# Optimization experiments

Hardware: AMD Instinct MI355X
Metric: run time of the kernel (lower is better)

The kernel has to match this reference:

```python
import jax, jax.numpy as jnp
import numpy as np

B, N, D, H = 512, 64, 3, 128


def setup_inputs() -> dict:
    key = jax.random.key(0)
    ks = jax.random.split(key, 7)
    s1 = 1.0 / np.sqrt(6.0)
    s2 = 1.0 / np.sqrt(float(H))
    return {
        "pos_scaled": jax.random.normal(ks[0], (B, N, D), dtype=jnp.float32),
        "W1": jax.random.normal(ks[1], (6, H), dtype=jnp.float32) * s1,
        "b1": jax.random.normal(ks[2], (H,), dtype=jnp.float32) * 0.01,
        "W2": jax.random.normal(ks[3], (H, H), dtype=jnp.float32) * s2,
        "b2": jax.random.normal(ks[4], (H,), dtype=jnp.float32) * 0.01,
        "W3": jax.random.normal(ks[5], (H, 1), dtype=jnp.float32) * s2,
        "b3": jax.random.normal(ks[6], (1,), dtype=jnp.float32) * 0.01,
    }


def _features(dist):
    # dist: [B, N, N, 1]
    inv_r = 1.0 / jnp.maximum(dist, 0.5)
    inv6 = inv_r ** 6
    return jnp.concatenate(
        [dist, inv_r, inv6, inv6 * inv6, inv6 * inv_r, inv6 * inv6 * inv_r], axis=-1
    )  # [B, N, N, 6]


def reference(pos_scaled, W1, b1, W2, b2, W3, b3):
    # all-pairs displacement: [B, N, N, D]
    diff = pos_scaled[:, :, None, :] - pos_scaled[:, None, :, :]
    sq = jnp.sum(diff * diff, axis=-1, keepdims=True)  # [B, N, N, 1]
    # safe sqrt (grad-safe at 0; forward value identical)
    dist = jnp.sqrt(jnp.where(sq > 0, sq, 1.0))
    dist = jnp.where(sq > 0, dist, 0.0)

    feat = _features(dist)  # [B, N, N, 6]
    h = jnp.tanh(feat @ W1 + b1)
    h = jnp.tanh(h @ W2 + b2)
    mag = h @ W3 + b3  # [B, N, N, 1]

    n = pos_scaled.shape[1]
    mask = (~jnp.eye(n, dtype=bool))[None, :, :, None]  # off-diagonal pairs
    direction = diff / jnp.maximum(dist, 0.01)
    pair_forces = jnp.where(mask, mag * direction, 0.0)
    return jnp.sum(pair_forces, axis=2)  # [B, N, D]
```

## Files before the change

kernel.cpp:

```cpp
#include <hip/hip_runtime.h>
#include <hip/hip_bf16.h>
#include <math.h>


#define NFINE   16384
#define NCOARSE 8192
#define ENTRIES 128
#define NBUILD  ((NFINE + NCOARSE) / ENTRIES)

typedef __attribute__((ext_vector_type(8))) short bf16x8;
typedef __attribute__((ext_vector_type(4))) float f32x4;
typedef __attribute__((ext_vector_type(8))) unsigned short ushort8_t;

__device__ __forceinline__ float fast_tanh(float x) {
    float e = __expf(2.0f * x);
    return 1.0f - 2.0f * __builtin_amdgcn_rcpf(e + 1.0f);
}

__device__ __forceinline__ unsigned short f2bf(float x) {
    __hip_bfloat16 h = __float2bfloat16(x);
    return *reinterpret_cast<unsigned short*>(&h);
}

__global__ __launch_bounds__(256) void build_table(
    const float* __restrict__ W1, const float* __restrict__ b1,
    const float* __restrict__ W2, const float* __restrict__ b2,
    const float* __restrict__ W3, const float* __restrict__ b3,
    float* __restrict__ tabF, float* __restrict__ tabC) {
    __shared__ __attribute__((aligned(16))) float sW1[6 * 128];
    __shared__ __attribute__((aligned(16))) float sb1[128], sb2[128], sW3[128];
    __shared__ __attribute__((aligned(16))) unsigned short sW2T[128][136];

    const int t = threadIdx.x;

    if (t < 128) { sb1[t] = b1[t]; sb2[t] = b2[t]; sW3[t] = W3[t]; }
    for (int i = t; i < 768; i += 256) sW1[i] = W1[i];

    {
        int q = t & 63, c = t >> 6;
        const float* r0 = W2 + (2 * q) * 128 + c * 32;
        const float* r1 = r0 + 128;
#pragma unroll
        for (int m = 0; m < 8; ++m) {
            float4 a = *reinterpret_cast<const float4*>(r0 + 4 * m);
            float4 b = *reinterpret_cast<const float4*>(r1 + 4 * m);
            int n = c * 32 + 4 * m;
            *reinterpret_cast<ushort2*>(&sW2T[n + 0][2 * q]) = make_ushort2(f2bf(a.x), f2bf(b.x));
            *reinterpret_cast<ushort2*>(&sW2T[n + 1][2 * q]) = make_ushort2(f2bf(a.y), f2bf(b.y));
            *reinterpret_cast<ushort2*>(&sW2T[n + 2][2 * q]) = make_ushort2(f2bf(a.z), f2bf(b.z));
            *reinterpret_cast<ushort2*>(&sW2T[n + 3][2 * q]) = make_ushort2(f2bf(a.w), f2bf(b.w));
        }
    }

    int eb = blockIdx.x * ENTRIES;
    float dd; float* tp; int lo;
    if (eb < NFINE) { dd = 2.0f / (float)NFINE;    tp = tabF; lo = eb; }
    else            { dd = 16.0f / (float)NCOARSE; tp = tabC; lo = eb - NFINE; }

    const int w  = t >> 6;
    const int l  = t & 63;
    const int lg = l >> 4;
    const int lr = l & 15;

    __syncthreads();

    const float b3v = b3[0];

#pragma unroll
    for (int et = 0; et < 2; ++et) {
        const int e = et * 64 + w * 16 + lr;
        float d = (float)(lo + e) * dd;
        float inv_r = 1.0f / fmaxf(d, 0.5f);
        float inv2  = inv_r * inv_r;
        float inv6  = inv2 * inv2 * inv2;
        float inv12 = inv6 * inv6;
        float ft[6] = {d, inv_r, inv6, inv12, inv6 * inv_r, inv12 * inv_r};

        bf16x8 afr[4];
#pragma unroll
        for (int kt = 0; kt < 4; ++kt) {
            int c0 = kt * 32 + lg * 8;
            float ac[8], wv[8];
            *reinterpret_cast<float4*>(&ac[0]) = *reinterpret_cast<const float4*>(&sb1[c0]);
            *reinterpret_cast<float4*>(&ac[4]) = *reinterpret_cast<const float4*>(&sb1[c0 + 4]);
#pragma unroll
            for (int k = 0; k < 6; ++k) {
                *reinterpret_cast<float4*>(&wv[0]) = *reinterpret_cast<const float4*>(&sW1[k * 128 + c0]);
                *reinterpret_cast<float4*>(&wv[4]) = *reinterpret_cast<const float4*>(&sW1[k * 128 + c0 + 4]);
#pragma unroll
                for (int j = 0; j < 8; ++j) ac[j] = fmaf(ft[k], wv[j], ac[j]);
            }
            ushort8_t pk;
#pragma unroll
            for (int j = 0; j < 8; ++j) pk[j] = f2bf(fast_tanh(ac[j]));
            afr[kt] = *reinterpret_cast<bf16x8*>(&pk);
        }

        float part[4] = {0.f, 0.f, 0.f, 0.f};
#pragma unroll
        for (int nt = 0; nt < 8; ++nt) {
            f32x4 acc = {0.f, 0.f, 0.f, 0.f};
#pragma unroll
            for (int kt = 0; kt < 4; ++kt) {
                bf16x8 bfr = *reinterpret_cast<const bf16x8*>(&sW2T[nt * 16 + lr][kt * 32 + lg * 8]);
                acc = __builtin_amdgcn_mfma_f32_16x16x32_bf16(afr[kt], bfr, acc, 0, 0, 0);
            }
            float b2v = sb2[nt * 16 + lr];
            float w3v = sW3[nt * 16 + lr];
#pragma unroll
            for (int r = 0; r < 4; ++r)
                part[r] = fmaf(fast_tanh(acc[r] + b2v), w3v, part[r]);
        }
#pragma unroll
        for (int s = 1; s < 16; s <<= 1) {
#pragma unroll
            for (int r = 0; r < 4; ++r) part[r] += __shfl_xor(part[r], s);
        }
        if (lr == 0) {
            int ebase = et * 64 + w * 16 + lg * 4;
#pragma unroll
            for (int r = 0; r < 4; ++r) {
                int ee = lo + ebase + r;
                float dr = (float)ee * dd;
                tp[ee] = (part[r] + b3v) / fmaxf(dr, 0.01f);
            }
        }
    }
}

__global__ __launch_bounds__(256) void force_kernel(
    const float* __restrict__ pos, const float* __restrict__ tabF,
    const float* __restrict__ tabC, float* __restrict__ out) {
    __shared__ float sp[192];
    int b = blockIdx.x;
    int t = threadIdx.x;
    if (t < 192) sp[t] = pos[b * 192 + t];
    __syncthreads();

    int i  = t >> 2;
    int j0 = (t & 3) * 16;
    float xi = sp[i * 3 + 0], yi = sp[i * 3 + 1], zi = sp[i * 3 + 2];
    float fx = 0.f, fy = 0.f, fz = 0.f;
#pragma unroll
    for (int jj = 0; jj < 16; ++jj) {
        int j = j0 + jj;
        float dx = xi - sp[j * 3 + 0];
        float dy = yi - sp[j * 3 + 1];
        float dz = zi - sp[j * 3 + 2];
        float sq = fmaf(dx, dx, fmaf(dy, dy, dz * dz));
        float dist = sqrtf(sq);

        bool fine = dist < 2.0f;
        const float* tb = fine ? tabF : tabC;
        float scale = fine ? ((float)NFINE / 2.0f) : ((float)NCOARSE / 16.0f);
        int tmax = fine ? NFINE : NCOARSE;
        float tpos = dist * scale;
        int i0 = min((int)tpos, tmax - 2);
        float fr = tpos - (float)i0;
        float g0 = tb[i0], g1 = tb[i0 + 1];
        float g = fmaf(fr, g1 - g0, g0);
        if (j == i) g = 0.0f;

        fx = fmaf(g, dx, fx);
        fy = fmaf(g, dy, fy);
        fz = fmaf(g, dz, fz);
    }
    fx += __shfl_xor(fx, 1); fy += __shfl_xor(fy, 1); fz += __shfl_xor(fz, 1);
    fx += __shfl_xor(fx, 2); fy += __shfl_xor(fy, 2); fz += __shfl_xor(fz, 2);
    if ((t & 3) == 0) {
        int o = (b * 64 + i) * 3;
        out[o + 0] = fx;
        out[o + 1] = fy;
        out[o + 2] = fz;
    }
}

extern "C" void kernel_launch(void* const* d_in, const int* in_sizes, int n_in,
                              void* d_out, int out_size, void* d_ws, size_t ws_size,
                              hipStream_t stream) {
    const float* pos = (const float*)d_in[0];
    const float* W1  = (const float*)d_in[1];
    const float* b1  = (const float*)d_in[2];
    const float* W2  = (const float*)d_in[3];
    const float* b2  = (const float*)d_in[4];
    const float* W3  = (const float*)d_in[5];
    const float* b3  = (const float*)d_in[6];

    char* ws = (char*)d_ws;
    float* tabF = (float*)(ws);
    float* tabC = (float*)(ws + (size_t)NFINE * 4);
    float* out = (float*)d_out;

    hipLaunchKernelGGL(build_table, dim3(NBUILD), dim3(256), 0, stream,
                       W1, b1, W2, b2, W3, b3, tabF, tabC);
    hipLaunchKernelGGL(force_kernel, dim3(512), dim3(256), 0, stream,
                       pos, tabF, tabC, out);
}
```

Measured before the change: 19.38 us.

## Exploit pair antisymmetry with shuffles, one wavefront per system

The force kernel now assigns one wavefront per 64-particle system and four systems per block. Each lane evaluates only half the pairs, using the cyclic offset m=1..32, and receives the opposite-sign contribution for the mirrored pair from another lane through __shfl. This roughly halves the table lookups and sqrt work and removes the final cross-lane reduction. The cost is three extra shuffles per iteration and a quarter as many blocks, which lowers parallelism across CUs.

```diff
diff --git a/kernel.cpp b/kernel.cpp
--- a/kernel.cpp
+++ b/kernel.cpp
@@ -131,22 +131,25 @@
 __global__ __launch_bounds__(256) void force_kernel(
     const float* __restrict__ pos, const float* __restrict__ tabF,
     const float* __restrict__ tabC, float* __restrict__ out) {
-    __shared__ float sp[192];
-    int b = blockIdx.x;
+    __shared__ float sp[768];
     int t = threadIdx.x;
-    if (t < 192) sp[t] = pos[b * 192 + t];
+    int b4 = blockIdx.x * 768;
+    for (int idx = t; idx < 768; idx += 256) sp[idx] = pos[b4 + idx];
     __syncthreads();
 
-    int i  = t >> 2;
-    int j0 = (t & 3) * 16;
-    float xi = sp[i * 3 + 0], yi = sp[i * 3 + 1], zi = sp[i * 3 + 2];
+    int w = t >> 6;
+    int l = t & 63;
+    const float* p = sp + w * 192;
+
+    float xi = p[l * 3 + 0], yi = p[l * 3 + 1], zi = p[l * 3 + 2];
     float fx = 0.f, fy = 0.f, fz = 0.f;
-#pragma unroll
-    for (int jj = 0; jj < 16; ++jj) {
-        int j = j0 + jj;
-        float dx = xi - sp[j * 3 + 0];
-        float dy = yi - sp[j * 3 + 1];
-        float dz = zi - sp[j * 3 + 2];
+
+#pragma unroll 8
+    for (int m = 1; m <= 32; ++m) {
+        int j = (l + m) & 63;
+        float dx = xi - p[j * 3 + 0];
+        float dy = yi - p[j * 3 + 1];
+        float dz = zi - p[j * 3 + 2];
         float sq = fmaf(dx, dx, fmaf(dy, dy, dz * dz));
         float dist = sqrtf(sq);
 
@@ -159,20 +162,21 @@
         float fr = tpos - (float)i0;
         float g0 = tb[i0], g1 = tb[i0 + 1];
         float g = fmaf(fr, g1 - g0, g0);
-        if (j == i) g = 0.0f;
-
-        fx = fmaf(g, dx, fx);
-        fy = fmaf(g, dy, fy);
-        fz = fmaf(g, dz, fz);
+
+        float px = g * dx, py = g * dy, pz = g * dz;
+        fx += px; fy += py; fz += pz;
+        if (m < 32) {
+            int src = (l - m + 64) & 63;
+            fx -= __shfl(px, src);
+            fy -= __shfl(py, src);
+            fz -= __shfl(pz, src);
+        }
     }
-    fx += __shfl_xor(fx, 1); fy += __shfl_xor(fy, 1); fz += __shfl_xor(fz, 1);
-    fx += __shfl_xor(fx, 2); fy += __shfl_xor(fy, 2); fz += __shfl_xor(fz, 2);
-    if ((t & 3) == 0) {
-        int o = (b * 64 + i) * 3;
-        out[o + 0] = fx;
-        out[o + 1] = fy;
-        out[o + 2] = fz;
-    }
+
+    int o = (blockIdx.x * 4 + w) * 192 + l * 3;
+    out[o + 0] = fx;
+    out[o + 1] = fy;
+    out[o + 2] = fz;
 }
 
 extern "C" void kernel_launch(void* const* d_in, const int* in_sizes, int n_in,
@@ -193,6 +197,6 @@
 
     hipLaunchKernelGGL(build_table, dim3(NBUILD), dim3(256), 0, stream,
                        W1, b1, W2, b2, W3, b3, tabF, tabC);
-    hipLaunchKernelGGL(force_kernel, dim3(512), dim3(256), 0, stream,
+    hipLaunchKernelGGL(force_kernel, dim3(128), dim3(256), 0, stream,
                        pos, tabF, tabC, out);
 }
```

After: 21.58 us. +11.4%, slower.
